# Optimization experiments

Measured on AMD Instinct MI355X. Metric: run time of the kernel, lower is better.

## Reference

```python
import jax, jax.numpy as jnp
import numpy as np

B, N, H, L, R, E = 8, 10000, 64, 4, 3, 200000
FP, NUM_CELLS = 2048, 100
LN_EPS = 1e-3  # Keras LayerNormalization default epsilon


def setup_inputs() -> dict:
    key = jax.random.key(0)
    ks = jax.random.split(key, 24)
    g = lambda k, shape, fan: (jax.random.uniform(k, shape, jnp.float32) * 2 - 1) * np.sqrt(6.0 / fan)
    inp = {
        'ctl_expr': jax.random.normal(ks[0], (B, N), jnp.float32),
        'drug_targets': jax.random.uniform(ks[1], (B, N), jnp.float32),
        'drug_fp': jax.random.uniform(ks[2], (B, FP), jnp.float32),
        'edge_weight': jax.random.uniform(ks[3], (R, E), jnp.float32),
        'cell_idx': jax.random.randint(ks[4], (B,), 0, NUM_CELLS, jnp.int32),
        'edge_index': jax.random.randint(ks[5], (R, 2, E), 0, N, jnp.int32),
        # parameters
        'W_se': g(ks[6], (1, H), 1 + H),
        'b_se': jnp.zeros((H,), jnp.float32),
        'cell_emb': jax.random.normal(ks[7], (NUM_CELLS, H), jnp.float32) * 0.05,
        'W_f1': g(ks[8], (FP, H), FP + H),
        'b_f1': jnp.zeros((H,), jnp.float32),
        'W_f2': g(ks[9], (H, 2 * H), 3 * H) * 0.1,
        'b_f2': jnp.zeros((2 * H,), jnp.float32),
        'Wself': jnp.stack([g(ks[10 + l], (H, H), 2 * H) for l in range(L)]),
        'Wrel': jnp.stack([jnp.stack([g(jax.random.fold_in(ks[14], l * R + r), (H, H), 2 * H) for r in range(R)]) for l in range(L)]),
        'ln_g': jnp.ones((L, H), jnp.float32),
        'ln_b': jnp.zeros((L, H), jnp.float32),
        'W_out': g(ks[15], (H, 1), H + 1),
        'b_out': jnp.zeros((1,), jnp.float32),
    }
    return inp


def reference(ctl_expr, drug_targets, drug_fp, edge_weight, cell_idx, edge_index,
              W_se, b_se, cell_emb, W_f1, b_f1, W_f2, b_f2,
              Wself, Wrel, ln_g, ln_b, W_out, b_out):
    # shared_embedding: Dense(H, relu) applied to scalar node features
    def shared(v):  # v: [B,N] -> [B,N,H]
        return jax.nn.relu(v[..., None] * W_se[0] + b_se)

    x = shared(ctl_expr) + shared(drug_targets)            # [B,N,H]
    x = x + cell_emb[cell_idx][:, None, :]                 # cell embedding broadcast

    # drug FiLM: gamma/beta conditioning
    film = jax.nn.relu(drug_fp @ W_f1 + b_f1) @ W_f2 + b_f2  # [B,2H]
    gamma, beta = jnp.split(film, 2, axis=-1)
    gamma = jnp.tanh(gamma)
    x = x * (1.0 + gamma[:, None, :]) + beta[:, None, :]

    n_layers, n_rel = Wself.shape[0], Wrel.shape[1]
    for l in range(n_layers):
        out = x @ Wself[l]                                 # self projection [B,N,H]
        for r in range(n_rel):
            src, dst = edge_index[r, 0], edge_index[r, 1]
            h = x @ Wrel[l, r]                             # [B,N,H]
            msg = edge_weight[r][None, :, None] * h[:, src, :]  # [B,E,H]
            out = out.at[:, dst].add(msg)                  # scatter-add to dst nodes
        # LayerNorm over feature dim (Keras eps=1e-3)
        mu = out.mean(-1, keepdims=True)
        var = ((out - mu) ** 2).mean(-1, keepdims=True)
        out = (out - mu) * jax.lax.rsqrt(var + LN_EPS) * ln_g[l] + ln_b[l]
        x = jax.nn.relu(out)

    return (x @ W_out)[..., 0] + b_out[0]                  # [B,N]
```

## Files before the change

kernel.cpp:

```cpp
#include <hip/hip_runtime.h>
#include <hip/hip_bf16.h>
#include <math.h>

#define Bk 8
#define Nk 10000
#define Hk 64
#define Lk 4
#define Rk 3
#define Ek 200000
#define FPk 2048

#define C4 (Rk*Ek/4)
#define CNT4B ((C4 + 255)/256)
#define INITB 2048
#define DEGW  (Rk*Nk*16)

typedef unsigned short u16;
typedef unsigned int   u32;
typedef _Float16 f16;
typedef __attribute__((ext_vector_type(2))) _Float16 f16x2;
typedef __attribute__((ext_vector_type(8))) _Float16 f16x8;
typedef __attribute__((ext_vector_type(4))) float f32x4;

__device__ __forceinline__ f16x2 as_h2(u32 u){
    union{u32 i; f16x2 h;} v; v.i = u; return v.h;
}
__device__ __forceinline__ u32 as_u32(f16x2 h){
    union{u32 i; f16x2 h;} v; v.h = h; return v.i;
}
__device__ __forceinline__ u16 f2h_bits(float f){
    union{f16 h; u16 u;} v; v.h = (f16)f; return v.u;
}

__global__ void k_prep0(const float* __restrict__ Wself, const float* __restrict__ Wrel,
                        u16* __restrict__ wt, int* __restrict__ deg,
                        const float* __restrict__ fp, const float* __restrict__ W1,
                        const float* __restrict__ b1, float* __restrict__ hid){
    __shared__ float red[256];
    if(blockIdx.x < 256){
        int idx = blockIdx.x*256 + threadIdx.x;
        if(idx < DEGW/8){
            *(int4*)&deg[idx*8]     = make_int4(0,0,0,0);
            *(int4*)&deg[idx*8 + 4] = make_int4(0,0,0,0);
        }
        int j    = idx & 7;
        int lane = (idx >> 3) & 63;
        int jt   = (idx >> 9) & 3;
        int kc   = (idx >> 11) & 1;
        int mt   = (idx >> 12) & 3;
        int l    = idx >> 14;
        int k    = kc*32 + (lane >> 4)*8 + j;
        int col  = jt*16 + (lane & 15);
        float w = (mt == 0) ? Wself[(l*64 + k)*64 + col]
                            : Wrel[((l*3 + (mt-1))*64 + k)*64 + col];
        wt[idx] = f2h_bits(w);
    }else{
        int bb = blockIdx.x - 256;
        int b = bb >> 6, h = bb & 63;
        const float* fpb = fp + b*FPk;
        float acc = 0.f;
        for(int k = threadIdx.x; k < FPk; k += 256)
            acc += fpb[k] * W1[k*64 + h];
        red[threadIdx.x] = acc;
        __syncthreads();
        for(int s = 128; s >= 1; s >>= 1){
            if(threadIdx.x < s) red[threadIdx.x] += red[threadIdx.x + s];
            __syncthreads();
        }
        if(threadIdx.x == 0) hid[b*64 + h] = fmaxf(red[0] + b1[h], 0.f);
    }
}

__global__ void k_efill(const int* __restrict__ edge_index, const float* __restrict__ edge_weight,
                        int* __restrict__ deg, u32* __restrict__ epack){
    int idx = blockIdx.x*256 + threadIdx.x;
    if(idx >= C4) return;
    int g = idx*4;
    int r = g / Ek, e = g % Ek;
    int4   s4 = *(const int4*)  &edge_index [r*2*Ek + e];
    int4   d4 = *(const int4*)  &edge_index [r*2*Ek + Ek + e];
    float4 w4 = *(const float4*)&edge_weight[r*Ek + e];
    int* dg = deg + (size_t)r*Nk*16;
    size_t ebase = (size_t)r*Nk;
    int pos;
    pos = atomicAdd(&dg[(size_t)d4.x*16], 1);
    if(pos < 64) epack[((ebase + d4.x) << 6) + pos] = ((u32)f2h_bits(w4.x) << 16) | (u32)s4.x;
    pos = atomicAdd(&dg[(size_t)d4.y*16], 1);
    if(pos < 64) epack[((ebase + d4.y) << 6) + pos] = ((u32)f2h_bits(w4.y) << 16) | (u32)s4.y;
    pos = atomicAdd(&dg[(size_t)d4.z*16], 1);
    if(pos < 64) epack[((ebase + d4.z) << 6) + pos] = ((u32)f2h_bits(w4.z) << 16) | (u32)s4.z;
    pos = atomicAdd(&dg[(size_t)d4.w*16], 1);
    if(pos < 64) epack[((ebase + d4.w) << 6) + pos] = ((u32)f2h_bits(w4.w) << 16) | (u32)s4.w;
}

__global__ void k_xinit(const float* __restrict__ ctl, const float* __restrict__ dt,
                        const int* __restrict__ cell_idx,
                        const float* __restrict__ W_se, const float* __restrict__ b_se,
                        const float* __restrict__ cell_emb,
                        const float* __restrict__ hid, const float* __restrict__ W2,
                        const float* __restrict__ b2,
                        u16* __restrict__ xh){
    __shared__ float g1l[64], btl[64];
    int b   = blockIdx.x >> 8;
    int blk = blockIdx.x & 255;
    int t = threadIdx.x;
    if(t < 128){
        float acc = b2[t];
        #pragma unroll 8
        for(int k = 0; k < 64; ++k)
            acc += hid[b*64 + k] * W2[k*128 + t];
        if(t < 64) g1l[t] = 1.f + tanhf(acc);
        else       btl[t - 64] = acc;
    }
    __syncthreads();
    int ci = cell_idx[b];
    const int per_b = Nk*8;
    for(int o = blk*256 + t; o < per_b; o += 256*256){
        int hq = o & 7;
        int n  = o >> 3;
        float c = ctl[b*Nk + n], d = dt[b*Nk + n];
        u32 pk[4];
        #pragma unroll
        for(int j = 0; j < 8; j += 2){
            int h0 = hq*8 + j, h1 = h0 + 1;
            float w0 = W_se[h0], s0 = b_se[h0];
            float w1 = W_se[h1], s1 = b_se[h1];
            float v0 = fmaxf(c*w0 + s0, 0.f) + fmaxf(d*w0 + s0, 0.f)
                     + cell_emb[ci*64 + h0];
            float v1 = fmaxf(c*w1 + s1, 0.f) + fmaxf(d*w1 + s1, 0.f)
                     + cell_emb[ci*64 + h1];
            v0 = v0 * g1l[h0] + btl[h0];
            v1 = v1 * g1l[h1] + btl[h1];
            pk[j >> 1] = (u32)f2h_bits(v0) | ((u32)f2h_bits(v1) << 16);
        }
        *(int4*)&xh[(((size_t)b*Nk + n)*64) + hq*8] = make_int4(pk[0], pk[1], pk[2], pk[3]);
    }
}

__global__ __launch_bounds__(256) void k_agg(const u16* __restrict__ xh,
                      const int* __restrict__ deg, const u32* __restrict__ epack,
                      u16* __restrict__ aggh){
    __shared__ int2 stash[4][64];
    int bpair = blockIdx.x & 3;
    int grp   = blockIdx.x >> 2;
    int wq    = threadIdx.x >> 6;
    int wid   = grp*4 + wq;
    int lane  = threadIdx.x & 63;
    int fg    = lane & 31;
    int bl    = lane >> 5;
    int b     = bpair*2 + bl;
    int r = wid / Nk, dst = wid % Nk;
    int cnt = deg[(size_t)wid*16]; if(cnt > 64) cnt = 64;
    const u32* ep = epack + ((size_t)wid << 6);
    const char* xb = (const char*)xh + (size_t)b*Nk*128 + fg*4;

    f16x2 A = (f16x2){0,0}, C = (f16x2){0,0};
    int2* st = stash[wq];
    if(lane < cnt){
        u32 e = ep[lane];
        st[lane] = make_int2((int)((e & 0xFFFFu) << 7),
                             (int)((e >> 16) | (e & 0xFFFF0000u)));
    }
    int t = 0;
    for(; t + 8 <= cnt; t += 8){
        int4 q01 = *(const int4*)&st[t];
        int4 q23 = *(const int4*)&st[t+2];
        int4 q45 = *(const int4*)&st[t+4];
        int4 q67 = *(const int4*)&st[t+6];
        u32 u0 = *(const u32*)(xb + q01.x);
        u32 u1 = *(const u32*)(xb + q01.z);
        u32 u2 = *(const u32*)(xb + q23.x);
        u32 u3 = *(const u32*)(xb + q23.z);
        u32 u4 = *(const u32*)(xb + q45.x);
        u32 u5 = *(const u32*)(xb + q45.z);
        u32 u6 = *(const u32*)(xb + q67.x);
        u32 u7 = *(const u32*)(xb + q67.z);
        A += as_h2(u0)*as_h2(q01.y); C += as_h2(u1)*as_h2(q01.w);
        A += as_h2(u2)*as_h2(q23.y); C += as_h2(u3)*as_h2(q23.w);
        A += as_h2(u4)*as_h2(q45.y); C += as_h2(u5)*as_h2(q45.w);
        A += as_h2(u6)*as_h2(q67.y); C += as_h2(u7)*as_h2(q67.w);
    }
    for(; t + 2 <= cnt; t += 2){
        int4 q01 = *(const int4*)&st[t];
        u32 u0 = *(const u32*)(xb + q01.x);
        u32 u1 = *(const u32*)(xb + q01.z);
        A += as_h2(u0)*as_h2(q01.y); C += as_h2(u1)*as_h2(q01.w);
    }
    if(t < cnt){
        int2 p = st[t];
        u32 u = *(const u32*)(xb + p.x);
        A += as_h2(u)*as_h2(p.y);
    }
    float a0 = (float)A.x + (float)C.x;
    float a1 = (float)A.y + (float)C.y;
    u32 packed = (u32)f2h_bits(a0) | ((u32)f2h_bits(a1) << 16);
    ((u32*)aggh)[(((size_t)r*Bk + b)*Nk + dst)*32 + fg] = packed;
}

__global__ __launch_bounds__(256) void k_proj_mfma(u16* __restrict__ xh,
        const u16* __restrict__ aggh, const u16* __restrict__ wt,
        const float* __restrict__ ln_g, const float* __restrict__ ln_b, int l,
        int last, const float* __restrict__ W_out, const float* __restrict__ b_out,
        float* __restrict__ out){
    __shared__ u16 wls[16384];
    const u16* wl = wt + (size_t)l*16384;
    for(int i = threadIdx.x; i < 2048; i += 256)
        *(int4*)&wls[i*8] = *(const int4*)&wl[i*8];
    __syncthreads();

    int lane = threadIdx.x & 63;
    int wq   = threadIdx.x >> 6;
    int k8   = blockIdx.x & 7;
    int b    = ((k8 & 3) << 1) | (k8 >> 2);
    int tile = blockIdx.x >> 3;
    int n0   = tile*128 + wq*32;
    int mrow = lane & 15;
    int kq   = lane >> 4;
    int nA = n0 + mrow;       if(nA >= Nk) nA = Nk - 1;
    int nB = n0 + 16 + mrow;  if(nB >= Nk) nB = Nk - 1;

    f32x4 accA[4], accB[4];
    #pragma unroll
    for(int jt = 0; jt < 4; ++jt){
        accA[jt] = (f32x4){0.f,0.f,0.f,0.f};
        accB[jt] = (f32x4){0.f,0.f,0.f,0.f};
    }

    #pragma unroll
    for(int mt = 0; mt < 4; ++mt){
        const u16* basep = (mt == 0)
            ? xh   + (size_t)b*Nk*64
            : aggh + (((size_t)(mt-1)*Bk + b)*Nk)*64;
        const u16* arowA = basep + (size_t)nA*64;
        const u16* arowB = basep + (size_t)nB*64;
        #pragma unroll
        for(int kc = 0; kc < 2; ++kc){
            f16x8 aA = *(const f16x8*)(arowA + kc*32 + kq*8);
            f16x8 aB = *(const f16x8*)(arowB + kc*32 + kq*8);
            #pragma unroll
            for(int jt = 0; jt < 4; ++jt){
                f16x8 bfrag = *(const f16x8*)(wls + ((size_t)((mt*2 + kc)*4 + jt)*64 + lane)*8);
                accA[jt] = __builtin_amdgcn_mfma_f32_16x16x32_f16(aA, bfrag, accA[jt], 0, 0, 0);
                accB[jt] = __builtin_amdgcn_mfma_f32_16x16x32_f16(aB, bfrag, accB[jt], 0, 0, 0);
            }
        }
    }

    float gv[4], bv[4], wo[4];
    #pragma unroll
    for(int jt = 0; jt < 4; ++jt){
        int f = jt*16 + mrow;
        gv[jt] = ln_g[l*64 + f];
        bv[jt] = ln_b[l*64 + f];
        wo[jt] = W_out[f];
    }
    float bo = b_out[0];
    u16* xdst = xh + (size_t)b*Nk*64;

    #pragma unroll
    for(int half = 0; half < 2; ++half){
        f32x4* acc = half ? accB : accA;
        int nbase = n0 + half*16;
        #pragma unroll
        for(int v = 0; v < 4; ++v){
            float s1 = acc[0][v] + acc[1][v] + acc[2][v] + acc[3][v];
            float s2 = acc[0][v]*acc[0][v] + acc[1][v]*acc[1][v]
                     + acc[2][v]*acc[2][v] + acc[3][v]*acc[3][v];
            #pragma unroll
            for(int off = 1; off <= 8; off <<= 1){
                s1 += __shfl_xor(s1, off);
                s2 += __shfl_xor(s2, off);
            }
            float mu  = s1 * 0.015625f;
            float var = s2 * 0.015625f - mu*mu;
            float rstd = rsqrtf(var + 1e-3f);
            int node = nbase + kq*4 + v;
            if(!last){
                if(node < Nk){
                    #pragma unroll
                    for(int jt = 0; jt < 4; ++jt){
                        float o = (acc[jt][v] - mu) * rstd * gv[jt] + bv[jt];
                        xdst[(size_t)node*64 + jt*16 + mrow] = f2h_bits(fmaxf(o, 0.f));
                    }
                }
            }else{
                float s3 = 0.f;
                #pragma unroll
                for(int jt = 0; jt < 4; ++jt){
                    float o = (acc[jt][v] - mu) * rstd * gv[jt] + bv[jt];
                    s3 += fmaxf(o, 0.f) * wo[jt];
                }
                #pragma unroll
                for(int off = 1; off <= 8; off <<= 1)
                    s3 += __shfl_xor(s3, off);
                if(mrow == 0 && node < Nk)
                    out[(size_t)b*Nk + node] = s3 + bo;
            }
        }
    }
}

extern "C" void kernel_launch(void* const* d_in, const int* in_sizes, int n_in,
                              void* d_out, int out_size, void* d_ws, size_t ws_size,
                              hipStream_t stream){
    const float* ctl        = (const float*)d_in[0];
    const float* dt         = (const float*)d_in[1];
    const float* drug_fp    = (const float*)d_in[2];
    const float* edge_w     = (const float*)d_in[3];
    const int*   cell_idx   = (const int*)  d_in[4];
    const int*   edge_index = (const int*)  d_in[5];
    const float* W_se       = (const float*)d_in[6];
    const float* b_se       = (const float*)d_in[7];
    const float* cell_emb   = (const float*)d_in[8];
    const float* W_f1       = (const float*)d_in[9];
    const float* b_f1       = (const float*)d_in[10];
    const float* W_f2       = (const float*)d_in[11];
    const float* b_f2       = (const float*)d_in[12];
    const float* Wself      = (const float*)d_in[13];
    const float* Wrel       = (const float*)d_in[14];
    const float* ln_g       = (const float*)d_in[15];
    const float* ln_b       = (const float*)d_in[16];
    const float* W_out      = (const float*)d_in[17];
    const float* b_out      = (const float*)d_in[18];
    float* out = (float*)d_out;

    char* p = (char*)d_ws;
    auto alloc = [&](size_t bytes)->char*{
        char* r = p; p += (bytes + 255) & ~(size_t)255; return r;
    };
    int*   deg    = (int*)  alloc((size_t)DEGW*4);
    u32*   epack  = (u32*)  alloc((size_t)Rk*Nk*64*4);
    float* hid    = (float*)alloc((size_t)Bk*64*4);
    u16*   xh     = (u16*)  alloc((size_t)Bk*Nk*64*2);
    u16*   aggh   = (u16*)  alloc((size_t)3*Bk*Nk*64*2);
    u16*   wt     = (u16*)  alloc((size_t)Lk*16384*2);

    k_prep0<<<256 + Bk*64, 256, 0, stream>>>(Wself, Wrel, wt, deg,
                                             drug_fp, W_f1, b_f1, hid);
    k_efill<<<CNT4B, 256, 0, stream>>>(edge_index, edge_w, deg, epack);
    k_xinit<<<INITB, 256, 0, stream>>>(ctl, dt, cell_idx, W_se, b_se, cell_emb,
                                       hid, W_f2, b_f2, xh);

    const int ntile = (Nk + 127)/128;
    for(int l = 0; l < Lk; ++l){
        k_agg<<<4*7500, 256, 0, stream>>>(xh, deg, epack, aggh);
        k_proj_mfma<<<ntile*8, 256, 0, stream>>>(
            xh, aggh, wt, ln_g, ln_b, l,
            (l == Lk-1) ? 1 : 0, W_out, b_out, out);
    }
}
```

Baseline: 362.6 us.

## Pipeline aggregation and projection across batch halves in one fused layer kernel

Aggregation and projection are merged into one k_layer kernel and the batch is split into two halves. Each launch runs the projection of one half alongside the neighbour gather of the other half, so the memory-bound gather overlaps the MFMA projection instead of running serially. The edge-fill and x-init kernels are also merged into a single launch. The projection now reads its weight fragments straight from global memory instead of staging them in LDS, which may add cache traffic and adds block-scheduling imbalance between the two block roles.

Result: slower. 505.8 us (+39.5%).

```diff
diff --git a/kernel.cpp b/kernel.cpp
--- a/kernel.cpp
+++ b/kernel.cpp
@@ -15,6 +15,9 @@
 #define INITB 2048
 #define DEGW  (Rk*Nk*16)
 
+#define PROJB 320
+#define AGGB  15000
+
 typedef unsigned short u16;
 typedef unsigned int   u32;
 typedef _Float16 f16;
@@ -24,9 +27,6 @@
 
 __device__ __forceinline__ f16x2 as_h2(u32 u){
     union{u32 i; f16x2 h;} v; v.i = u; return v.h;
-}
-__device__ __forceinline__ u32 as_u32(f16x2 h){
-    union{u32 i; f16x2 h;} v; v.h = h; return v.i;
 }
 __device__ __forceinline__ u16 f2h_bits(float f){
     union{f16 h; u16 u;} v; v.h = (f16)f; return v.u;
@@ -71,29 +71,9 @@
     }
 }
 
-__global__ void k_efill(const int* __restrict__ edge_index, const float* __restrict__ edge_weight,
-                        int* __restrict__ deg, u32* __restrict__ epack){
-    int idx = blockIdx.x*256 + threadIdx.x;
-    if(idx >= C4) return;
-    int g = idx*4;
-    int r = g / Ek, e = g % Ek;
-    int4   s4 = *(const int4*)  &edge_index [r*2*Ek + e];
-    int4   d4 = *(const int4*)  &edge_index [r*2*Ek + Ek + e];
-    float4 w4 = *(const float4*)&edge_weight[r*Ek + e];
-    int* dg = deg + (size_t)r*Nk*16;
-    size_t ebase = (size_t)r*Nk;
-    int pos;
-    pos = atomicAdd(&dg[(size_t)d4.x*16], 1);
-    if(pos < 64) epack[((ebase + d4.x) << 6) + pos] = ((u32)f2h_bits(w4.x) << 16) | (u32)s4.x;
-    pos = atomicAdd(&dg[(size_t)d4.y*16], 1);
-    if(pos < 64) epack[((ebase + d4.y) << 6) + pos] = ((u32)f2h_bits(w4.y) << 16) | (u32)s4.y;
-    pos = atomicAdd(&dg[(size_t)d4.z*16], 1);
-    if(pos < 64) epack[((ebase + d4.z) << 6) + pos] = ((u32)f2h_bits(w4.z) << 16) | (u32)s4.z;
-    pos = atomicAdd(&dg[(size_t)d4.w*16], 1);
-    if(pos < 64) epack[((ebase + d4.w) << 6) + pos] = ((u32)f2h_bits(w4.w) << 16) | (u32)s4.w;
-}
-
-__global__ void k_xinit(const float* __restrict__ ctl, const float* __restrict__ dt,
+__global__ void k_fill2(const int* __restrict__ edge_index, const float* __restrict__ edge_weight,
+                        int* __restrict__ deg, u32* __restrict__ epack,
+                        const float* __restrict__ ctl, const float* __restrict__ dt,
                         const int* __restrict__ cell_idx,
                         const float* __restrict__ W_se, const float* __restrict__ b_se,
                         const float* __restrict__ cell_emb,
@@ -101,118 +81,140 @@
                         const float* __restrict__ b2,
                         u16* __restrict__ xh){
     __shared__ float g1l[64], btl[64];
-    int b   = blockIdx.x >> 8;
-    int blk = blockIdx.x & 255;
-    int t = threadIdx.x;
-    if(t < 128){
-        float acc = b2[t];
-        #pragma unroll 8
-        for(int k = 0; k < 64; ++k)
-            acc += hid[b*64 + k] * W2[k*128 + t];
-        if(t < 64) g1l[t] = 1.f + tanhf(acc);
-        else       btl[t - 64] = acc;
-    }
-    __syncthreads();
-    int ci = cell_idx[b];
-    const int per_b = Nk*8;
-    for(int o = blk*256 + t; o < per_b; o += 256*256){
-        int hq = o & 7;
-        int n  = o >> 3;
-        float c = ctl[b*Nk + n], d = dt[b*Nk + n];
-        u32 pk[4];
-        #pragma unroll
-        for(int j = 0; j < 8; j += 2){
-            int h0 = hq*8 + j, h1 = h0 + 1;
-            float w0 = W_se[h0], s0 = b_se[h0];
-            float w1 = W_se[h1], s1 = b_se[h1];
-            float v0 = fmaxf(c*w0 + s0, 0.f) + fmaxf(d*w0 + s0, 0.f)
-                     + cell_emb[ci*64 + h0];
-            float v1 = fmaxf(c*w1 + s1, 0.f) + fmaxf(d*w1 + s1, 0.f)
-                     + cell_emb[ci*64 + h1];
-            v0 = v0 * g1l[h0] + btl[h0];
-            v1 = v1 * g1l[h1] + btl[h1];
-            pk[j >> 1] = (u32)f2h_bits(v0) | ((u32)f2h_bits(v1) << 16);
-        }
-        *(int4*)&xh[(((size_t)b*Nk + n)*64) + hq*8] = make_int4(pk[0], pk[1], pk[2], pk[3]);
-    }
-}
-
-__global__ __launch_bounds__(256) void k_agg(const u16* __restrict__ xh,
-                      const int* __restrict__ deg, const u32* __restrict__ epack,
-                      u16* __restrict__ aggh){
+    if(blockIdx.x < CNT4B){
+        int idx = blockIdx.x*256 + threadIdx.x;
+        if(idx >= C4) return;
+        int g = idx*4;
+        int r = g / Ek, e = g % Ek;
+        int4   s4 = *(const int4*)  &edge_index [r*2*Ek + e];
+        int4   d4 = *(const int4*)  &edge_index [r*2*Ek + Ek + e];
+        float4 w4 = *(const float4*)&edge_weight[r*Ek + e];
+        int* dg = deg + (size_t)r*Nk*16;
+        size_t ebase = (size_t)r*Nk;
+        int pos;
+        pos = atomicAdd(&dg[(size_t)d4.x*16], 1);
+        if(pos < 64) epack[((ebase + d4.x) << 6) + pos] = ((u32)f2h_bits(w4.x) << 16) | (u32)s4.x;
+        pos = atomicAdd(&dg[(size_t)d4.y*16], 1);
+        if(pos < 64) epack[((ebase + d4.y) << 6) + pos] = ((u32)f2h_bits(w4.y) << 16) | (u32)s4.y;
+        pos = atomicAdd(&dg[(size_t)d4.z*16], 1);
+        if(pos < 64) epack[((ebase + d4.z) << 6) + pos] = ((u32)f2h_bits(w4.z) << 16) | (u32)s4.z;
+        pos = atomicAdd(&dg[(size_t)d4.w*16], 1);
+        if(pos < 64) epack[((ebase + d4.w) << 6) + pos] = ((u32)f2h_bits(w4.w) << 16) | (u32)s4.w;
+    }else{
+        int bb  = blockIdx.x - CNT4B;
+        int b   = bb >> 8;
+        int blk = bb & 255;
+        int t = threadIdx.x;
+        if(t < 128){
+            float acc = b2[t];
+            #pragma unroll 8
+            for(int k = 0; k < 64; ++k)
+                acc += hid[b*64 + k] * W2[k*128 + t];
+            if(t < 64) g1l[t] = 1.f + tanhf(acc);
+            else       btl[t - 64] = acc;
+        }
+        __syncthreads();
+        int ci = cell_idx[b];
+        const int per_b = Nk*8;
+        for(int o = blk*256 + t; o < per_b; o += 256*256){
+            int hq = o & 7;
+            int n  = o >> 3;
+            float c = ctl[b*Nk + n], d = dt[b*Nk + n];
+            u32 pk[4];
+            #pragma unroll
+            for(int j = 0; j < 8; j += 2){
+                int h0 = hq*8 + j, h1 = h0 + 1;
+                float w0 = W_se[h0], s0 = b_se[h0];
+                float w1 = W_se[h1], s1 = b_se[h1];
+                float v0 = fmaxf(c*w0 + s0, 0.f) + fmaxf(d*w0 + s0, 0.f)
+                         + cell_emb[ci*64 + h0];
+                float v1 = fmaxf(c*w1 + s1, 0.f) + fmaxf(d*w1 + s1, 0.f)
+                         + cell_emb[ci*64 + h1];
+                v0 = v0 * g1l[h0] + btl[h0];
+                v1 = v1 * g1l[h1] + btl[h1];
+                pk[j >> 1] = (u32)f2h_bits(v0) | ((u32)f2h_bits(v1) << 16);
+            }
+            *(int4*)&xh[(((size_t)b*Nk + n)*64) + hq*8] = make_int4(pk[0], pk[1], pk[2], pk[3]);
+        }
+    }
+}
+
+__global__ __launch_bounds__(256) void k_layer(
+        u16* __restrict__ xh, const int* __restrict__ deg,
+        const u32* __restrict__ epack, u16* __restrict__ aggh,
+        const u16* __restrict__ wt,
+        const float* __restrict__ ln_g, const float* __restrict__ ln_b,
+        int projL, int projHalf, int doProj, int last, int aggHalf,
+        const float* __restrict__ W_out, const float* __restrict__ b_out,
+        float* __restrict__ out){
     __shared__ int2 stash[4][64];
-    int bpair = blockIdx.x & 3;
-    int grp   = blockIdx.x >> 2;
-    int wq    = threadIdx.x >> 6;
-    int wid   = grp*4 + wq;
-    int lane  = threadIdx.x & 63;
-    int fg    = lane & 31;
-    int bl    = lane >> 5;
-    int b     = bpair*2 + bl;
-    int r = wid / Nk, dst = wid % Nk;
-    int cnt = deg[(size_t)wid*16]; if(cnt > 64) cnt = 64;
-    const u32* ep = epack + ((size_t)wid << 6);
-    const char* xb = (const char*)xh + (size_t)b*Nk*128 + fg*4;
-
-    f16x2 A = (f16x2){0,0}, C = (f16x2){0,0};
-    int2* st = stash[wq];
-    if(lane < cnt){
-        u32 e = ep[lane];
-        st[lane] = make_int2((int)((e & 0xFFFFu) << 7),
-                             (int)((e >> 16) | (e & 0xFFFF0000u)));
-    }
-    int t = 0;
-    for(; t + 8 <= cnt; t += 8){
-        int4 q01 = *(const int4*)&st[t];
-        int4 q23 = *(const int4*)&st[t+2];
-        int4 q45 = *(const int4*)&st[t+4];
-        int4 q67 = *(const int4*)&st[t+6];
-        u32 u0 = *(const u32*)(xb + q01.x);
-        u32 u1 = *(const u32*)(xb + q01.z);
-        u32 u2 = *(const u32*)(xb + q23.x);
-        u32 u3 = *(const u32*)(xb + q23.z);
-        u32 u4 = *(const u32*)(xb + q45.x);
-        u32 u5 = *(const u32*)(xb + q45.z);
-        u32 u6 = *(const u32*)(xb + q67.x);
-        u32 u7 = *(const u32*)(xb + q67.z);
-        A += as_h2(u0)*as_h2(q01.y); C += as_h2(u1)*as_h2(q01.w);
-        A += as_h2(u2)*as_h2(q23.y); C += as_h2(u3)*as_h2(q23.w);
-        A += as_h2(u4)*as_h2(q45.y); C += as_h2(u5)*as_h2(q45.w);
-        A += as_h2(u6)*as_h2(q67.y); C += as_h2(u7)*as_h2(q67.w);
-    }
-    for(; t + 2 <= cnt; t += 2){
-        int4 q01 = *(const int4*)&st[t];
-        u32 u0 = *(const u32*)(xb + q01.x);
-        u32 u1 = *(const u32*)(xb + q01.z);
-        A += as_h2(u0)*as_h2(q01.y); C += as_h2(u1)*as_h2(q01.w);
-    }
-    if(t < cnt){
-        int2 p = st[t];
-        u32 u = *(const u32*)(xb + p.x);
-        A += as_h2(u)*as_h2(p.y);
-    }
-    float a0 = (float)A.x + (float)C.x;
-    float a1 = (float)A.y + (float)C.y;
-    u32 packed = (u32)f2h_bits(a0) | ((u32)f2h_bits(a1) << 16);
-    ((u32*)aggh)[(((size_t)r*Bk + b)*Nk + dst)*32 + fg] = packed;
-}
-
-__global__ __launch_bounds__(256) void k_proj_mfma(u16* __restrict__ xh,
-        const u16* __restrict__ aggh, const u16* __restrict__ wt,
-        const float* __restrict__ ln_g, const float* __restrict__ ln_b, int l,
-        int last, const float* __restrict__ W_out, const float* __restrict__ b_out,
-        float* __restrict__ out){
-    __shared__ u16 wls[16384];
-    const u16* wl = wt + (size_t)l*16384;
-    for(int i = threadIdx.x; i < 2048; i += 256)
-        *(int4*)&wls[i*8] = *(const int4*)&wl[i*8];
-    __syncthreads();
-
+
+    if(blockIdx.x >= PROJB){
+        int agg_id = blockIdx.x - PROJB;
+        int bpl  = agg_id & 1;
+        int grp  = agg_id >> 1;
+        int wq   = threadIdx.x >> 6;
+        int wid  = grp*4 + wq;
+        int lane = threadIdx.x & 63;
+        int fg   = lane & 31;
+        int bl   = lane >> 5;
+        int b    = aggHalf*4 + bpl*2 + bl;
+        int r = wid / Nk, dst = wid % Nk;
+        int cnt = deg[(size_t)wid*16]; if(cnt > 64) cnt = 64;
+        const u32* ep = epack + ((size_t)wid << 6);
+        const char* xb = (const char*)xh + (size_t)b*Nk*128 + fg*4;
+
+        f16x2 A = (f16x2){0,0}, C = (f16x2){0,0};
+        int2* st = stash[wq];
+        if(lane < cnt){
+            u32 e = ep[lane];
+            st[lane] = make_int2((int)((e & 0xFFFFu) << 7),
+                                 (int)((e >> 16) | (e & 0xFFFF0000u)));
+        }
+        int t = 0;
+        for(; t + 8 <= cnt; t += 8){
+            int4 q01 = *(const int4*)&st[t];
+            int4 q23 = *(const int4*)&st[t+2];
+            int4 q45 = *(const int4*)&st[t+4];
+            int4 q67 = *(const int4*)&st[t+6];
+            u32 u0 = *(const u32*)(xb + q01.x);
+            u32 u1 = *(const u32*)(xb + q01.z);
+            u32 u2 = *(const u32*)(xb + q23.x);
+            u32 u3 = *(const u32*)(xb + q23.z);
+            u32 u4 = *(const u32*)(xb + q45.x);
+            u32 u5 = *(const u32*)(xb + q45.z);
+            u32 u6 = *(const u32*)(xb + q67.x);
+            u32 u7 = *(const u32*)(xb + q67.z);
+            A += as_h2(u0)*as_h2(q01.y); C += as_h2(u1)*as_h2(q01.w);
+            A += as_h2(u2)*as_h2(q23.y); C += as_h2(u3)*as_h2(q23.w);
+            A += as_h2(u4)*as_h2(q45.y); C += as_h2(u5)*as_h2(q45.w);
+            A += as_h2(u6)*as_h2(q67.y); C += as_h2(u7)*as_h2(q67.w);
+        }
+        for(; t + 2 <= cnt; t += 2){
+            int4 q01 = *(const int4*)&st[t];
+            u32 u0 = *(const u32*)(xb + q01.x);
+            u32 u1 = *(const u32*)(xb + q01.z);
+            A += as_h2(u0)*as_h2(q01.y); C += as_h2(u1)*as_h2(q01.w);
+        }
+        if(t < cnt){
+            int2 p = st[t];
+            u32 u = *(const u32*)(xb + p.x);
+            A += as_h2(u)*as_h2(p.y);
+        }
+        float a0 = (float)A.x + (float)C.x;
+        float a1 = (float)A.y + (float)C.y;
+        u32 packed = (u32)f2h_bits(a0) | ((u32)f2h_bits(a1) << 16);
+        ((u32*)aggh)[(((size_t)r*Bk + b)*Nk + dst)*32 + fg] = packed;
+        return;
+    }
+
+    if(!doProj) return;
+    int p = blockIdx.x;
+    int tile = p >> 2;
+    if(tile >= 79) return;
+    int b    = projHalf*4 + (p & 3);
     int lane = threadIdx.x & 63;
     int wq   = threadIdx.x >> 6;
-    int k8   = blockIdx.x & 7;
-    int b    = ((k8 & 3) << 1) | (k8 >> 2);
-    int tile = blockIdx.x >> 3;
     int n0   = tile*128 + wq*32;
     int mrow = lane & 15;
     int kq   = lane >> 4;
@@ -225,6 +227,8 @@
         accA[jt] = (f32x4){0.f,0.f,0.f,0.f};
         accB[jt] = (f32x4){0.f,0.f,0.f,0.f};
     }
+
+    const u16* wl = wt + (size_t)projL*16384;
 
     #pragma unroll
     for(int mt = 0; mt < 4; ++mt){
@@ -239,7 +243,7 @@
             f16x8 aB = *(const f16x8*)(arowB + kc*32 + kq*8);
             #pragma unroll
             for(int jt = 0; jt < 4; ++jt){
-                f16x8 bfrag = *(const f16x8*)(wls + ((size_t)((mt*2 + kc)*4 + jt)*64 + lane)*8);
+                f16x8 bfrag = *(const f16x8*)(wl + ((size_t)((mt*2 + kc)*4 + jt)*64 + lane)*8);
                 accA[jt] = __builtin_amdgcn_mfma_f32_16x16x32_f16(aA, bfrag, accA[jt], 0, 0, 0);
                 accB[jt] = __builtin_amdgcn_mfma_f32_16x16x32_f16(aB, bfrag, accB[jt], 0, 0, 0);
             }
@@ -250,8 +254,8 @@
     #pragma unroll
     for(int jt = 0; jt < 4; ++jt){
         int f = jt*16 + mrow;
-        gv[jt] = ln_g[l*64 + f];
-        bv[jt] = ln_b[l*64 + f];
+        gv[jt] = ln_g[projL*64 + f];
+        bv[jt] = ln_b[projL*64 + f];
         wo[jt] = W_out[f];
     }
     float bo = b_out[0];
@@ -337,15 +341,22 @@
 
     k_prep0<<<256 + Bk*64, 256, 0, stream>>>(Wself, Wrel, wt, deg,
                                              drug_fp, W_f1, b_f1, hid);
-    k_efill<<<CNT4B, 256, 0, stream>>>(edge_index, edge_w, deg, epack);
-    k_xinit<<<INITB, 256, 0, stream>>>(ctl, dt, cell_idx, W_se, b_se, cell_emb,
-                                       hid, W_f2, b_f2, xh);
-
-    const int ntile = (Nk + 127)/128;
+    k_fill2<<<CNT4B + INITB, 256, 0, stream>>>(edge_index, edge_w, deg, epack,
+                                               ctl, dt, cell_idx, W_se, b_se, cell_emb,
+                                               hid, W_f2, b_f2, xh);
+
+    k_layer<<<PROJB + AGGB, 256, 0, stream>>>(xh, deg, epack, aggh, wt, ln_g, ln_b,
+            0, 0, 0, 0, 0, W_out, b_out, out);
     for(int l = 0; l < Lk; ++l){
-        k_agg<<<4*7500, 256, 0, stream>>>(xh, deg, epack, aggh);
-        k_proj_mfma<<<ntile*8, 256, 0, stream>>>(
-            xh, aggh, wt, ln_g, ln_b, l,
-            (l == Lk-1) ? 1 : 0, W_out, b_out, out);
-    }
-}
+        k_layer<<<PROJB + AGGB, 256, 0, stream>>>(xh, deg, epack, aggh, wt, ln_g, ln_b,
+                l, 0, 1, (l == Lk-1) ? 1 : 0, 1,
+                W_out, b_out, out);
+        if(l < Lk-1)
+            k_layer<<<PROJB + AGGB, 256, 0, stream>>>(xh, deg, epack, aggh, wt, ln_g, ln_b,
+                    l, 1, 1, 0, 0,
+                    W_out, b_out, out);
+    }
+    k_layer<<<PROJB, 256, 0, stream>>>(xh, deg, epack, aggh, wt, ln_g, ln_b,
+            Lk-1, 1, 1, 1, 0,
+            W_out, b_out, out);
+}
```
